# Kernel optimization log

Measured on AMD Instinct MI355X. Metric: run time of the kernel, lower is better.

The kernel has to match this reference:

```python
import jax, jax.numpy as jnp
import numpy as np
from functools import partial

ALPHA = 0.1
THETA = 0.5
N_NODES = 100000
N_EDGES = 3200000


def _gcn_norm(edge_index, num_nodes):
    # add self loops, compute symmetric normalization D^-1/2 (A+I) D^-1/2
    loops = jnp.arange(num_nodes, dtype=edge_index.dtype)
    src = jnp.concatenate([edge_index[0], loops])
    dst = jnp.concatenate([edge_index[1], loops])
    deg = jax.ops.segment_sum(jnp.ones_like(dst, dtype=jnp.float32), dst,
                              num_segments=num_nodes)
    dinv = jnp.where(deg > 0, jax.lax.rsqrt(deg), 0.0)
    norm = dinv[src] * dinv[dst]  # [E+N]
    return src, dst, norm


def _propagate(h, src, dst, norm, num_nodes):
    # out[i] = sum_{e: dst[e]=i} norm[e] * h[src[e]]
    msg = h[src] * norm[:, None]
    return jax.ops.segment_sum(msg, dst, num_segments=num_nodes)


def setup_inputs() -> dict:
    key = jax.random.key(0)
    ks = jax.random.split(key, 7)
    H, Fin, Fout, L = 256, 512, 64, 8
    x = jax.random.normal(ks[0], (N_NODES, Fin), dtype=jnp.float32)
    edge_index = jax.random.randint(ks[1], (2, N_EDGES), 0, N_NODES, dtype=jnp.int64)
    s = 1.0 / np.sqrt(Fin)
    W0 = jax.random.normal(ks[2], (Fin, H), dtype=jnp.float32) * s
    b0 = jax.random.normal(ks[3], (H,), dtype=jnp.float32) * 0.01
    Ws = jax.random.normal(ks[4], (L, H, H), dtype=jnp.float32) / np.sqrt(H)
    Wc = jax.random.normal(ks[5], (H, Fout), dtype=jnp.float32) / np.sqrt(H)
    bc = jax.random.normal(ks[6], (Fout,), dtype=jnp.float32) * 0.01
    return {"x": x, "edge_index": edge_index, "W0": W0, "b0": b0,
            "Ws": Ws, "Wc": Wc, "bc": bc}


def reference(x, edge_index, W0, b0, Ws, Wc, bc):
    num_nodes = x.shape[0]
    src, dst, norm = _gcn_norm(edge_index, num_nodes)
    # initial projection (dropout is identity in eval mode)
    x0 = jax.nn.relu(x @ W0 + b0)  # [N, H]
    h = x0
    layer_num = Ws.shape[0]
    for i in range(layer_num):
        beta = float(np.log(THETA / (i + 1) + 1.0))
        agg = _propagate(h, src, dst, norm, num_nodes)          # Ahat @ h
        z = (1.0 - ALPHA) * agg + ALPHA * x0                    # initial residual
        h = jax.nn.relu((1.0 - beta) * z + beta * (z @ Ws[i]))  # identity mapping
    embedding = h
    logits = embedding @ Wc + bc
    soft_label = jax.nn.softmax(logits, axis=1)
    hard_label = jnp.argmax(soft_label, axis=1)
    return logits, embedding, soft_label, hard_label
```

## Files before the change

### kernel.cpp

```cpp
#include <hip/hip_runtime.h>
#include <hip/hip_bf16.h>
#include <math.h>

#define NN   100000
#define FIN  512
#define HH   256
#define FOUT 64

typedef __attribute__((ext_vector_type(8))) short s16x8;
typedef __attribute__((ext_vector_type(4))) float f32x4;

__global__ void k_count(const int* __restrict__ dst, int* __restrict__ cnt, int E) {
    int i = blockIdx.x * 256 + threadIdx.x;
    if (i < E) atomicAdd(&cnt[dst[i]], 1);
}

__global__ void k_block_sums(const int* __restrict__ cnt, int* __restrict__ partial, int n) {
    __shared__ int red[256];
    int base = blockIdx.x * 1024;
    int t = threadIdx.x;
    int s = 0;
#pragma unroll
    for (int i = 0; i < 4; i++) { int idx = base + t * 4 + i; if (idx < n) s += cnt[idx]; }
    red[t] = s; __syncthreads();
    for (int off = 128; off > 0; off >>= 1) {
        if (t < off) red[t] += red[t + off];
        __syncthreads();
    }
    if (t == 0) partial[blockIdx.x] = red[0];
}

__global__ void k_scan_partials(int* partial, int nb, int* row_ptr, int n) {
    if (threadIdx.x == 0) {
        int run = 0;
        for (int i = 0; i < nb; i++) { int v = partial[i]; partial[i] = run; run += v; }
        row_ptr[n] = run;
    }
}

__global__ void k_write_rowptr(const int* __restrict__ cnt, const int* __restrict__ partial,
                               int* __restrict__ row_ptr, int* __restrict__ cur, int n) {
    __shared__ int sc[256];
    int base = blockIdx.x * 1024;
    int t = threadIdx.x;
    int v[4]; int s = 0;
#pragma unroll
    for (int i = 0; i < 4; i++) { int idx = base + t * 4 + i; v[i] = (idx < n) ? cnt[idx] : 0; s += v[i]; }
    sc[t] = s; __syncthreads();
    for (int off = 1; off < 256; off <<= 1) {
        int add = (t >= off) ? sc[t - off] : 0;
        __syncthreads();
        sc[t] += add;
        __syncthreads();
    }
    int run = partial[blockIdx.x] + sc[t] - s;
#pragma unroll
    for (int i = 0; i < 4; i++) {
        int idx = base + t * 4 + i;
        if (idx < n) { row_ptr[idx] = run; cur[idx] = run; run += v[i]; }
    }
}

__global__ void k_dinv(const int* __restrict__ cnt, float* __restrict__ dinv, int n) {
    int i = blockIdx.x * 256 + threadIdx.x;
    if (i < n) dinv[i] = 1.0f / sqrtf((float)(cnt[i] + 1));
}

__global__ void k_scatter(const int* __restrict__ src, const int* __restrict__ dst,
                          const float* __restrict__ dinv, int* __restrict__ cur,
                          int* __restrict__ src_sorted, float* __restrict__ norm_sorted, int E) {
    int i = blockIdx.x * 256 + threadIdx.x;
    if (i < E) {
        int s = src[i], d = dst[i];
        int p = atomicAdd(&cur[d], 1);
        src_sorted[p] = s;
        norm_sorted[p] = dinv[s] * dinv[d];
    }
}

__device__ __forceinline__ short f2bf_rn(float f) {
    unsigned b = __float_as_uint(f);
    unsigned r = b + 0x7FFFu + ((b >> 16) & 1u);
    return (short)(r >> 16);
}
__device__ __forceinline__ float bf2f(short h) {
    return __uint_as_float(((unsigned)(unsigned short)h) << 16);
}
__device__ __forceinline__ void split_bf16(float f, short& hi, short& lo) {
    hi = f2bf_rn(f);
    lo = f2bf_rn(f - bf2f(hi));
}

__global__ void k_wprep(const float* __restrict__ W, short* __restrict__ whi,
                        short* __restrict__ wlo, int K, float scale, int addId) {
    int t = blockIdx.x * 256 + threadIdx.x;
    int total = K * HH / 8;
    if (t >= total) return;
    int colin = t & 15, g = (t >> 4) & 3, nt = (t >> 6) & 15, kt = t >> 10;
    int col = nt * 16 + colin, kb = kt * 32 + g * 8;
    s16x8 h8, l8;
#pragma unroll
    for (int j = 0; j < 8; j++) {
        float f = scale * W[(size_t)(kb + j) * HH + col];
        if (addId && (kb + j) == col) f += 1.0f - scale;
        short h, l; split_bf16(f, h, l);
        h8[j] = h; l8[j] = l;
    }
    *(s16x8*)&whi[(size_t)t * 8] = h8;
    *(s16x8*)&wlo[(size_t)t * 8] = l8;
}

__global__ __launch_bounds__(256) void k_gemm0(
    const float* __restrict__ A, const short* __restrict__ Whi, const short* __restrict__ Wlo,
    const float* __restrict__ bias, float* __restrict__ C, int M) {
    __shared__ short As_hi[2][2048];
    __shared__ short As_lo[2][2048];
    int tid = threadIdx.x, lane = tid & 63, wid = tid >> 6;
    int wm = wid >> 1, wn = wid & 1;
    int bm = blockIdx.x * 64;
    int st_row = tid >> 2, st_g = tid & 3;
    int st_cphys = ((st_row & 15) ^ ((st_g & 1) << 2)) + 16 * st_g + 64 * (st_row >> 4);
    const float* st_ap = A + (size_t)(bm + st_row) * FIN + st_g * 8;
    bool st_ok = (bm + st_row) < M;
    int fr_g = lane >> 4, fr_r = lane & 15;
    int fr_base = (fr_r ^ ((fr_g & 1) << 2)) + 16 * fr_g;
    int c0 = (fr_base + 64 * (wm * 2 + 0)) * 8;
    int c1 = (fr_base + 64 * (wm * 2 + 1)) * 8;
    int lane_off = fr_g * 16 + fr_r;
    f32x4 acc[2][8] = {};
    f32x4 v0 = {0.f, 0.f, 0.f, 0.f}, v1 = v0, n0 = v0, n1 = v0;
    if (st_ok) { v0 = *(const f32x4*)(st_ap); v1 = *(const f32x4*)(st_ap + 4); }
    for (int kt = 0; kt < FIN / 32; kt++) {
        int buf = kt & 1;
        s16x8 h8, l8;
        {
            float fv[8] = {v0.x, v0.y, v0.z, v0.w, v1.x, v1.y, v1.z, v1.w};
#pragma unroll
            for (int j = 0; j < 8; j++) { short hh, ll; split_bf16(fv[j], hh, ll); h8[j] = hh; l8[j] = ll; }
        }
        *(s16x8*)&As_hi[buf][st_cphys * 8] = h8;
        *(s16x8*)&As_lo[buf][st_cphys * 8] = l8;
        if (kt + 1 < FIN / 32 && st_ok) {
            int k0n = (kt + 1) * 32;
            n0 = *(const f32x4*)(st_ap + k0n);
            n1 = *(const f32x4*)(st_ap + k0n + 4);
        }
        __syncthreads();
        s16x8 ah0 = *(const s16x8*)&As_hi[buf][c0], al0 = *(const s16x8*)&As_lo[buf][c0];
        s16x8 ah1 = *(const s16x8*)&As_hi[buf][c1], al1 = *(const s16x8*)&As_lo[buf][c1];
        size_t btile = (size_t)kt * 1024 + (size_t)(wn * 8) * 64;
#pragma unroll
        for (int ct = 0; ct < 8; ct++) {
            s16x8 bh = *(const s16x8*)&Whi[(btile + ct * 64 + lane_off) * 8];
            s16x8 bl = *(const s16x8*)&Wlo[(btile + ct * 64 + lane_off) * 8];
            acc[0][ct] = __builtin_amdgcn_mfma_f32_16x16x32_bf16(ah0, bh, acc[0][ct], 0, 0, 0);
            acc[0][ct] = __builtin_amdgcn_mfma_f32_16x16x32_bf16(al0, bh, acc[0][ct], 0, 0, 0);
            acc[0][ct] = __builtin_amdgcn_mfma_f32_16x16x32_bf16(ah0, bl, acc[0][ct], 0, 0, 0);
            acc[1][ct] = __builtin_amdgcn_mfma_f32_16x16x32_bf16(ah1, bh, acc[1][ct], 0, 0, 0);
            acc[1][ct] = __builtin_amdgcn_mfma_f32_16x16x32_bf16(al1, bh, acc[1][ct], 0, 0, 0);
            acc[1][ct] = __builtin_amdgcn_mfma_f32_16x16x32_bf16(ah1, bl, acc[1][ct], 0, 0, 0);
        }
        v0 = n0; v1 = n1;
    }
    int rsub = (lane >> 4) * 4, csub = lane & 15;
#pragma unroll
    for (int rt = 0; rt < 2; rt++)
#pragma unroll
        for (int ct = 0; ct < 8; ct++) {
            int col = wn * 128 + ct * 16 + csub;
            int r0 = bm + wm * 32 + rt * 16 + rsub;
#pragma unroll
            for (int reg = 0; reg < 4; reg++) {
                int row = r0 + reg;
                if (row < M) {
                    float o = fmaxf(acc[rt][ct][reg] + bias[col], 0.f);
                    C[(size_t)(col >> 7) * ((size_t)M * 128) + (size_t)row * 128 + (col & 127)] = o;
                }
            }
        }
}

__global__ __launch_bounds__(256) void k_prop(
    const float* __restrict__ hc, const float* __restrict__ x0c,
    const int* __restrict__ row_ptr, const int* __restrict__ src_sorted,
    const float* __restrict__ norm_sorted, const float* __restrict__ dinv,
    float* __restrict__ zc, int M) {
    int wid = threadIdx.x >> 6, lane = threadIdx.x & 63;
    int node = blockIdx.x * 4 + wid;
    if (node >= M) return;
    int slot = lane >> 5, f4 = (lane & 31) * 4;
    int e0 = __builtin_amdgcn_readfirstlane(row_ptr[node]);
    int e1 = __builtin_amdgcn_readfirstlane(row_ptr[node + 1]);
    f32x4 acc = {0.f, 0.f, 0.f, 0.f};
    int e = e0 + slot;
    for (; e + 2 < e1; e += 4) {
        int s0 = src_sorted[e];     float w0 = norm_sorted[e];
        int s1 = src_sorted[e + 2]; float w1 = norm_sorted[e + 2];
        f32x4 v0 = *(const f32x4*)&hc[(size_t)s0 * 128 + f4];
        f32x4 v1 = *(const f32x4*)&hc[(size_t)s1 * 128 + f4];
        acc += w0 * v0 + w1 * v1;
    }
    if (e < e1) {
        int s0 = src_sorted[e]; float w0 = norm_sorted[e];
        acc += w0 * (*(const f32x4*)&hc[(size_t)s0 * 128 + f4]);
    }
#pragma unroll
    for (int c = 0; c < 4; c++) acc[c] += __shfl_xor(acc[c], 32);
    float di = dinv[node], sw = di * di;
    size_t base = (size_t)node * 128 + f4;
    f32x4 hrow = *(const f32x4*)&hc[base];
    f32x4 xv = *(const f32x4*)&x0c[base];
    f32x4 z = 0.9f * (acc + sw * hrow) + 0.1f * xv;
    if (slot == 0) *(f32x4*)&zc[base] = z;
}

__global__ __launch_bounds__(256) void k_mgemm_z(
    const float* __restrict__ Zc, const short* __restrict__ Whi, const short* __restrict__ Wlo,
    float* __restrict__ C, int M, int rowmajor) {
    __shared__ short As_hi[2][2048];
    __shared__ short As_lo[2][2048];
    int tid = threadIdx.x, lane = tid & 63, wid = tid >> 6;
    int wm = wid >> 1, wn = wid & 1;
    int bm = blockIdx.x * 64;
    size_t CS = (size_t)M * 128;
    int st_row = tid >> 2, st_g = tid & 3;
    int st_cphys = ((st_row & 15) ^ ((st_g & 1) << 2)) + 16 * st_g + 64 * (st_row >> 4);
    bool st_ok = (bm + st_row) < M;
    int fr_g = lane >> 4, fr_r = lane & 15;
    int fr_base = (fr_r ^ ((fr_g & 1) << 2)) + 16 * fr_g;
    int c0 = (fr_base + 64 * (wm * 2 + 0)) * 8;
    int c1 = (fr_base + 64 * (wm * 2 + 1)) * 8;
    int lane_off = fr_g * 16 + fr_r;
    f32x4 acc[2][8] = {};
    auto zslab = [&](int kt) {
        int k0 = kt * 32;
        return Zc + (size_t)(k0 >> 7) * CS + (size_t)(bm + st_row) * 128 + (k0 & 127) + st_g * 8;
    };
    f32x4 v0 = {0.f, 0.f, 0.f, 0.f}, v1 = v0, n0 = v0, n1 = v0;
    if (st_ok) { const float* zp = zslab(0); v0 = *(const f32x4*)zp; v1 = *(const f32x4*)(zp + 4); }
    for (int kt = 0; kt < 8; kt++) {
        int buf = kt & 1;
        s16x8 h8, l8;
        {
            float fv[8] = {v0.x, v0.y, v0.z, v0.w, v1.x, v1.y, v1.z, v1.w};
#pragma unroll
            for (int j = 0; j < 8; j++) { short hh, ll; split_bf16(fv[j], hh, ll); h8[j] = hh; l8[j] = ll; }
        }
        *(s16x8*)&As_hi[buf][st_cphys * 8] = h8;
        *(s16x8*)&As_lo[buf][st_cphys * 8] = l8;
        if (kt + 1 < 8 && st_ok) {
            const float* zp = zslab(kt + 1);
            n0 = *(const f32x4*)zp; n1 = *(const f32x4*)(zp + 4);
        }
        __syncthreads();
        s16x8 ah0 = *(const s16x8*)&As_hi[buf][c0], al0 = *(const s16x8*)&As_lo[buf][c0];
        s16x8 ah1 = *(const s16x8*)&As_hi[buf][c1], al1 = *(const s16x8*)&As_lo[buf][c1];
        size_t btile = (size_t)kt * 1024 + (size_t)(wn * 8) * 64;
#pragma unroll
        for (int ct = 0; ct < 8; ct++) {
            s16x8 bh = *(const s16x8*)&Whi[(btile + ct * 64 + lane_off) * 8];
            s16x8 bl = *(const s16x8*)&Wlo[(btile + ct * 64 + lane_off) * 8];
            acc[0][ct] = __builtin_amdgcn_mfma_f32_16x16x32_bf16(ah0, bh, acc[0][ct], 0, 0, 0);
            acc[0][ct] = __builtin_amdgcn_mfma_f32_16x16x32_bf16(al0, bh, acc[0][ct], 0, 0, 0);
            acc[0][ct] = __builtin_amdgcn_mfma_f32_16x16x32_bf16(ah0, bl, acc[0][ct], 0, 0, 0);
            acc[1][ct] = __builtin_amdgcn_mfma_f32_16x16x32_bf16(ah1, bh, acc[1][ct], 0, 0, 0);
            acc[1][ct] = __builtin_amdgcn_mfma_f32_16x16x32_bf16(al1, bh, acc[1][ct], 0, 0, 0);
            acc[1][ct] = __builtin_amdgcn_mfma_f32_16x16x32_bf16(ah1, bl, acc[1][ct], 0, 0, 0);
        }
        v0 = n0; v1 = n1;
    }
    int rsub = (lane >> 4) * 4, csub = lane & 15;
#pragma unroll
    for (int rt = 0; rt < 2; rt++)
#pragma unroll
        for (int ct = 0; ct < 8; ct++) {
            int col = wn * 128 + ct * 16 + csub;
            int r0 = bm + wm * 32 + rt * 16 + rsub;
#pragma unroll
            for (int reg = 0; reg < 4; reg++) {
                int row = r0 + reg;
                if (row < M) {
                    float o = fmaxf(acc[rt][ct][reg], 0.f);
                    if (rowmajor) C[(size_t)row * HH + col] = o;
                    else C[(size_t)(col >> 7) * CS + (size_t)row * 128 + (col & 127)] = o;
                }
            }
        }
}

__global__ __launch_bounds__(256) void k_final2(
    const float* __restrict__ h, const float* __restrict__ Wc, const float* __restrict__ bc,
    float* __restrict__ logits, float* __restrict__ soft, float* __restrict__ hard, int M) {
    __shared__ float As[16][64];
    __shared__ float Bs[16][64];
    __shared__ float lg[64][64];
    int tid = threadIdx.x;
    int tx = tid & 15, ty = tid >> 4;
    int bm = blockIdx.x * 64;
    int lm = tid >> 2, lk = (tid & 3) * 4;
    int lkb = tid >> 4, lnb = (tid & 15) * 4;
    bool arow_ok = (bm + lm) < M;
    float acc[4][4] = {};
    for (int k0 = 0; k0 < HH; k0 += 16) {
        float4 av = make_float4(0.f, 0.f, 0.f, 0.f);
        if (arow_ok) av = *(const float4*)&h[(size_t)(bm + lm) * HH + k0 + lk];
        As[lk + 0][lm] = av.x; As[lk + 1][lm] = av.y; As[lk + 2][lm] = av.z; As[lk + 3][lm] = av.w;
        *(float4*)&Bs[lkb][lnb] = *(const float4*)&Wc[(size_t)(k0 + lkb) * FOUT + lnb];
        __syncthreads();
#pragma unroll
        for (int k = 0; k < 16; k++) {
            float4 a = *(const float4*)&As[k][ty * 4];
            float4 b = *(const float4*)&Bs[k][tx * 4];
            acc[0][0] += a.x * b.x; acc[0][1] += a.x * b.y; acc[0][2] += a.x * b.z; acc[0][3] += a.x * b.w;
            acc[1][0] += a.y * b.x; acc[1][1] += a.y * b.y; acc[1][2] += a.y * b.z; acc[1][3] += a.y * b.w;
            acc[2][0] += a.z * b.x; acc[2][1] += a.z * b.y; acc[2][2] += a.z * b.z; acc[2][3] += a.z * b.w;
            acc[3][0] += a.w * b.x; acc[3][1] += a.w * b.y; acc[3][2] += a.w * b.z; acc[3][3] += a.w * b.w;
        }
        __syncthreads();
    }
#pragma unroll
    for (int i = 0; i < 4; i++)
        *(float4*)&lg[ty * 4 + i][tx * 4] = make_float4(acc[i][0], acc[i][1], acc[i][2], acc[i][3]);
    __syncthreads();

    int wid = tid >> 6, lane = tid & 63;
    float bv = bc[lane];
    for (int r = wid * 16; r < wid * 16 + 16; r++) {
        int node = bm + r;
        if (node >= M) continue;
        float v = lg[r][lane] + bv;
        float m = v;
        for (int off = 32; off > 0; off >>= 1) m = fmaxf(m, __shfl_xor(m, off));
        float ev = expf(v - m);
        float s = ev;
        for (int off = 32; off > 0; off >>= 1) s += __shfl_xor(s, off);
        float sm = ev / s;
        int idx = lane; float vv = v;
        for (int off = 1; off < 64; off <<= 1) {
            float ov = __shfl_xor(vv, off);
            int oi = __shfl_xor(idx, off);
            if (ov > vv || (ov == vv && oi < idx)) { vv = ov; idx = oi; }
        }
        logits[(size_t)node * FOUT + lane] = v;
        soft[(size_t)node * FOUT + lane] = sm;
        if (lane == 0) hard[node] = (float)idx;
    }
}

extern "C" void kernel_launch(void* const* d_in, const int* in_sizes, int n_in,
                              void* d_out, int out_size, void* d_ws, size_t ws_size,
                              hipStream_t stream) {
    const float* x  = (const float*)d_in[0];
    const int*   ei = (const int*)d_in[1];
    const float* W0 = (const float*)d_in[2];
    const float* b0 = (const float*)d_in[3];
    const float* Ws = (const float*)d_in[4];
    const float* Wc = (const float*)d_in[5];
    const float* bc = (const float*)d_in[6];
    const int E = in_sizes[1] / 2;
    const int N = in_sizes[0] / FIN;
    const int L = in_sizes[4] / (HH * HH);

    float* out    = (float*)d_out;
    float* logits = out;
    float* emb    = out + (size_t)N * FOUT;
    float* soft   = emb + (size_t)N * HH;
    float* hard   = soft + (size_t)N * FOUT;

    char* p = (char*)d_ws;
    size_t off = 0;
    auto alloc = [&](size_t bytes) { void* r = p + off; off += (bytes + 255) & ~(size_t)255; return r; };
    int*   cnt         = (int*)alloc((size_t)N * 4);
    int*   row_ptr     = (int*)alloc((size_t)(N + 1) * 4);
    int*   cur         = (int*)alloc((size_t)N * 4);
    int*   partial     = (int*)alloc(4096 * 4);
    float* dinv        = (float*)alloc((size_t)N * 4);
    int*   src_sorted  = (int*)alloc((size_t)E * 4);
    float* norm_sorted = (float*)alloc((size_t)E * 4);
    float* X0c         = (float*)alloc((size_t)N * HH * 4);
    float* hAc         = (float*)alloc((size_t)N * HH * 4);
    float* hBc         = (float*)alloc((size_t)N * HH * 4);
    short* W0hi        = (short*)alloc((size_t)FIN * HH * 2);
    short* W0lo        = (short*)alloc((size_t)FIN * HH * 2);
    short* Wshi        = (short*)alloc((size_t)L * HH * HH * 2);
    short* Wslo        = (short*)alloc((size_t)L * HH * HH * 2);

    const int* srcp = ei;
    const int* dstp = ei + E;
    const size_t CS = (size_t)N * 128;

    hipMemsetAsync(cnt, 0, (size_t)N * 4, stream);
    k_count<<<(E + 255) / 256, 256, 0, stream>>>(dstp, cnt, E);
    const int nb = (N + 1023) / 1024;
    k_block_sums<<<nb, 256, 0, stream>>>(cnt, partial, N);
    k_scan_partials<<<1, 64, 0, stream>>>(partial, nb, row_ptr, N);
    k_write_rowptr<<<nb, 256, 0, stream>>>(cnt, partial, row_ptr, cur, N);
    k_dinv<<<(N + 255) / 256, 256, 0, stream>>>(cnt, dinv, N);
    k_scatter<<<(E + 255) / 256, 256, 0, stream>>>(srcp, dstp, dinv, cur, src_sorted, norm_sorted, E);

    k_wprep<<<(FIN * HH / 8 + 255) / 256, 256, 0, stream>>>(W0, W0hi, W0lo, FIN, 1.0f, 0);
    for (int i = 0; i < L; i++) {
        float beta = (float)log(0.5 / (i + 1) + 1.0);
        k_wprep<<<(HH * HH / 8 + 255) / 256, 256, 0, stream>>>(
            Ws + (size_t)i * HH * HH, Wshi + (size_t)i * HH * HH, Wslo + (size_t)i * HH * HH,
            HH, beta, 1);
    }

    const int nblk = (N + 63) / 64;
    const int npb  = (N + 3) / 4;
    k_gemm0<<<nblk, 256, 0, stream>>>(x, W0hi, W0lo, b0, X0c, N);

    const float* hsrc = X0c;
    for (int i = 0; i < L; i++) {
        int last = (i == L - 1);
        float* hdst = last ? emb : ((i & 1) ? hBc : hAc);
        float* zb = last ? hBc : hdst;
        for (int c = 0; c < 2; c++)
            k_prop<<<npb, 256, 0, stream>>>(hsrc + c * CS, X0c + c * CS, row_ptr,
                                            src_sorted, norm_sorted, dinv, zb + c * CS, N);
        k_mgemm_z<<<nblk, 256, 0, stream>>>(zb, Wshi + (size_t)i * HH * HH, Wslo + (size_t)i * HH * HH,
                                            hdst, N, last);
        hsrc = hdst;
    }
    k_final2<<<nblk, 256, 0, stream>>>(emb, Wc, bc, logits, soft, hard, N);
}
```

Measured before the change: 4.995 ms.

## Split GEMM tiles across 8 waves and batch weight prep into one launch

The two MFMA GEMM kernels go from 256 to 512 threads per block, so each wave owns a 32x64 output slice instead of 32x128, halving its accumulator registers. Only the first 256 threads stage A into shared memory, and a second barrier per k-step is added to protect the double buffer. The per-layer weight-prep launches are merged into one kernel that computes beta on the device. The aim is more waves in flight and fewer launches, at the cost of extra barriers and idle staging threads.

After: 4.840 ms. 1.03x faster.

```diff
diff --git a/kernel.cpp b/kernel.cpp
--- a/kernel.cpp
+++ b/kernel.cpp
@@ -92,7 +92,7 @@
 }
 
 __global__ void k_wprep(const float* __restrict__ W, short* __restrict__ whi,
-                        short* __restrict__ wlo, int K, float scale, int addId) {
+                        short* __restrict__ wlo, int K) {
     int t = blockIdx.x * 256 + threadIdx.x;
     int total = K * HH / 8;
     if (t >= total) return;
@@ -101,8 +101,7 @@
     s16x8 h8, l8;
 #pragma unroll
     for (int j = 0; j < 8; j++) {
-        float f = scale * W[(size_t)(kb + j) * HH + col];
-        if (addId && (kb + j) == col) f += 1.0f - scale;
+        float f = W[(size_t)(kb + j) * HH + col];
         short h, l; split_bf16(f, h, l);
         h8[j] = h; l8[j] = l;
     }
@@ -110,47 +109,70 @@
     *(s16x8*)&wlo[(size_t)t * 8] = l8;
 }
 
-__global__ __launch_bounds__(256) void k_gemm0(
+__global__ void k_wprep_all(const float* __restrict__ Ws, short* __restrict__ whi,
+                            short* __restrict__ wlo, int L) {
+    int t = blockIdx.x * 256 + threadIdx.x;
+    const int per = HH * HH / 8;
+    if (t >= L * per) return;
+    int layer = t / per;
+    int tl = t - layer * per;
+    float beta = (float)log(0.5 / (layer + 1) + 1.0);
+    const float* W = Ws + (size_t)layer * HH * HH;
+    int colin = tl & 15, g = (tl >> 4) & 3, nt = (tl >> 6) & 15, kt = tl >> 10;
+    int col = nt * 16 + colin, kb = kt * 32 + g * 8;
+    s16x8 h8, l8;
+#pragma unroll
+    for (int j = 0; j < 8; j++) {
+        float f = beta * W[(size_t)(kb + j) * HH + col];
+        if ((kb + j) == col) f += 1.0f - beta;
+        short h, l; split_bf16(f, h, l);
+        h8[j] = h; l8[j] = l;
+    }
+    *(s16x8*)&whi[(size_t)t * 8] = h8;
+    *(s16x8*)&wlo[(size_t)t * 8] = l8;
+}
+
+__global__ __launch_bounds__(512, 4) void k_gemm0(
     const float* __restrict__ A, const short* __restrict__ Whi, const short* __restrict__ Wlo,
     const float* __restrict__ bias, float* __restrict__ C, int M) {
     __shared__ short As_hi[2][2048];
     __shared__ short As_lo[2][2048];
     int tid = threadIdx.x, lane = tid & 63, wid = tid >> 6;
-    int wm = wid >> 1, wn = wid & 1;
+    int wm = wid >> 2, wn = wid & 3;
     int bm = blockIdx.x * 64;
     int st_row = tid >> 2, st_g = tid & 3;
     int st_cphys = ((st_row & 15) ^ ((st_g & 1) << 2)) + 16 * st_g + 64 * (st_row >> 4);
     const float* st_ap = A + (size_t)(bm + st_row) * FIN + st_g * 8;
-    bool st_ok = (bm + st_row) < M;
+    bool st_ok = (tid < 256) && (bm + st_row) < M;
     int fr_g = lane >> 4, fr_r = lane & 15;
     int fr_base = (fr_r ^ ((fr_g & 1) << 2)) + 16 * fr_g;
     int c0 = (fr_base + 64 * (wm * 2 + 0)) * 8;
     int c1 = (fr_base + 64 * (wm * 2 + 1)) * 8;
     int lane_off = fr_g * 16 + fr_r;
-    f32x4 acc[2][8] = {};
+    f32x4 acc[2][4] = {};
     f32x4 v0 = {0.f, 0.f, 0.f, 0.f}, v1 = v0, n0 = v0, n1 = v0;
     if (st_ok) { v0 = *(const f32x4*)(st_ap); v1 = *(const f32x4*)(st_ap + 4); }
     for (int kt = 0; kt < FIN / 32; kt++) {
         int buf = kt & 1;
-        s16x8 h8, l8;
-        {
+        if (tid < 256) {
+            s16x8 h8, l8;
             float fv[8] = {v0.x, v0.y, v0.z, v0.w, v1.x, v1.y, v1.z, v1.w};
 #pragma unroll
             for (int j = 0; j < 8; j++) { short hh, ll; split_bf16(fv[j], hh, ll); h8[j] = hh; l8[j] = ll; }
-        }
-        *(s16x8*)&As_hi[buf][st_cphys * 8] = h8;
-        *(s16x8*)&As_lo[buf][st_cphys * 8] = l8;
-        if (kt + 1 < FIN / 32 && st_ok) {
-            int k0n = (kt + 1) * 32;
-            n0 = *(const f32x4*)(st_ap + k0n);
-            n1 = *(const f32x4*)(st_ap + k0n + 4);
+            *(s16x8*)&As_hi[buf][st_cphys * 8] = h8;
+            *(s16x8*)&As_lo[buf][st_cphys * 8] = l8;
+            if (kt + 1 < FIN / 32 && st_ok) {
+                int k0n = (kt + 1) * 32;
+                n0 = *(const f32x4*)(st_ap + k0n);
+                n1 = *(const f32x4*)(st_ap + k0n + 4);
+            }
         }
         __syncthreads();
         s16x8 ah0 = *(const s16x8*)&As_hi[buf][c0], al0 = *(const s16x8*)&As_lo[buf][c0];
         s16x8 ah1 = *(const s16x8*)&As_hi[buf][c1], al1 = *(const s16x8*)&As_lo[buf][c1];
-        size_t btile = (size_t)kt * 1024 + (size_t)(wn * 8) * 64;
-#pragma unroll
-        for (int ct = 0; ct < 8; ct++) {
+        size_t btile = (size_t)kt * 1024 + (size_t)(wn * 4) * 64;
+#pragma unroll
+        for (int ct = 0; ct < 4; ct++) {
             s16x8 bh = *(const s16x8*)&Whi[(btile + ct * 64 + lane_off) * 8];
             s16x8 bl = *(const s16x8*)&Wlo[(btile + ct * 64 + lane_off) * 8];
             acc[0][ct] = __builtin_amdgcn_mfma_f32_16x16x32_bf16(ah0, bh, acc[0][ct], 0, 0, 0);
@@ -161,13 +183,14 @@
             acc[1][ct] = __builtin_amdgcn_mfma_f32_16x16x32_bf16(ah1, bl, acc[1][ct], 0, 0, 0);
         }
         v0 = n0; v1 = n1;
+        if (kt + 1 < FIN / 32) __syncthreads();
     }
     int rsub = (lane >> 4) * 4, csub = lane & 15;
 #pragma unroll
     for (int rt = 0; rt < 2; rt++)
 #pragma unroll
-        for (int ct = 0; ct < 8; ct++) {
-            int col = wn * 128 + ct * 16 + csub;
+        for (int ct = 0; ct < 4; ct++) {
+            int col = wn * 64 + ct * 16 + csub;
             int r0 = bm + wm * 32 + rt * 16 + rsub;
 #pragma unroll
             for (int reg = 0; reg < 4; reg++) {
@@ -214,24 +237,24 @@
     if (slot == 0) *(f32x4*)&zc[base] = z;
 }
 
-__global__ __launch_bounds__(256) void k_mgemm_z(
+__global__ __launch_bounds__(512, 4) void k_mgemm_z(
     const float* __restrict__ Zc, const short* __restrict__ Whi, const short* __restrict__ Wlo,
     float* __restrict__ C, int M, int rowmajor) {
     __shared__ short As_hi[2][2048];
     __shared__ short As_lo[2][2048];
     int tid = threadIdx.x, lane = tid & 63, wid = tid >> 6;
-    int wm = wid >> 1, wn = wid & 1;
+    int wm = wid >> 2, wn = wid & 3;
     int bm = blockIdx.x * 64;
     size_t CS = (size_t)M * 128;
     int st_row = tid >> 2, st_g = tid & 3;
+    bool st_ok = (tid < 256) && (bm + st_row) < M;
     int st_cphys = ((st_row & 15) ^ ((st_g & 1) << 2)) + 16 * st_g + 64 * (st_row >> 4);
-    bool st_ok = (bm + st_row) < M;
     int fr_g = lane >> 4, fr_r = lane & 15;
     int fr_base = (fr_r ^ ((fr_g & 1) << 2)) + 16 * fr_g;
     int c0 = (fr_base + 64 * (wm * 2 + 0)) * 8;
     int c1 = (fr_base + 64 * (wm * 2 + 1)) * 8;
     int lane_off = fr_g * 16 + fr_r;
-    f32x4 acc[2][8] = {};
+    f32x4 acc[2][4] = {};
     auto zslab = [&](int kt) {
         int k0 = kt * 32;
         return Zc + (size_t)(k0 >> 7) * CS + (size_t)(bm + st_row) * 128 + (k0 & 127) + st_g * 8;
@@ -240,24 +263,24 @@
     if (st_ok) { const float* zp = zslab(0); v0 = *(const f32x4*)zp; v1 = *(const f32x4*)(zp + 4); }
     for (int kt = 0; kt < 8; kt++) {
         int buf = kt & 1;
-        s16x8 h8, l8;
-        {
+        if (tid < 256) {
+            s16x8 h8, l8;
             float fv[8] = {v0.x, v0.y, v0.z, v0.w, v1.x, v1.y, v1.z, v1.w};
 #pragma unroll
             for (int j = 0; j < 8; j++) { short hh, ll; split_bf16(fv[j], hh, ll); h8[j] = hh; l8[j] = ll; }
-        }
-        *(s16x8*)&As_hi[buf][st_cphys * 8] = h8;
-        *(s16x8*)&As_lo[buf][st_cphys * 8] = l8;
-        if (kt + 1 < 8 && st_ok) {
-            const float* zp = zslab(kt + 1);
-            n0 = *(const f32x4*)zp; n1 = *(const f32x4*)(zp + 4);
+            *(s16x8*)&As_hi[buf][st_cphys * 8] = h8;
+            *(s16x8*)&As_lo[buf][st_cphys * 8] = l8;
+            if (kt + 1 < 8 && st_ok) {
+                const float* zp = zslab(kt + 1);
+                n0 = *(const f32x4*)zp; n1 = *(const f32x4*)(zp + 4);
+            }
         }
         __syncthreads();
         s16x8 ah0 = *(const s16x8*)&As_hi[buf][c0], al0 = *(const s16x8*)&As_lo[buf][c0];
         s16x8 ah1 = *(const s16x8*)&As_hi[buf][c1], al1 = *(const s16x8*)&As_lo[buf][c1];
-        size_t btile = (size_t)kt * 1024 + (size_t)(wn * 8) * 64;
-#pragma unroll
-        for (int ct = 0; ct < 8; ct++) {
+        size_t btile = (size_t)kt * 1024 + (size_t)(wn * 4) * 64;
+#pragma unroll
+        for (int ct = 0; ct < 4; ct++) {
             s16x8 bh = *(const s16x8*)&Whi[(btile + ct * 64 + lane_off) * 8];
             s16x8 bl = *(const s16x8*)&Wlo[(btile + ct * 64 + lane_off) * 8];
             acc[0][ct] = __builtin_amdgcn_mfma_f32_16x16x32_bf16(ah0, bh, acc[0][ct], 0, 0, 0);
@@ -268,13 +291,14 @@
             acc[1][ct] = __builtin_amdgcn_mfma_f32_16x16x32_bf16(ah1, bl, acc[1][ct], 0, 0, 0);
         }
         v0 = n0; v1 = n1;
+        if (kt + 1 < 8) __syncthreads();
     }
     int rsub = (lane >> 4) * 4, csub = lane & 15;
 #pragma unroll
     for (int rt = 0; rt < 2; rt++)
 #pragma unroll
-        for (int ct = 0; ct < 8; ct++) {
-            int col = wn * 128 + ct * 16 + csub;
+        for (int ct = 0; ct < 4; ct++) {
+            int col = wn * 64 + ct * 16 + csub;
             int r0 = bm + wm * 32 + rt * 16 + rsub;
 #pragma unroll
             for (int reg = 0; reg < 4; reg++) {
@@ -398,17 +422,12 @@
     k_dinv<<<(N + 255) / 256, 256, 0, stream>>>(cnt, dinv, N);
     k_scatter<<<(E + 255) / 256, 256, 0, stream>>>(srcp, dstp, dinv, cur, src_sorted, norm_sorted, E);
 
-    k_wprep<<<(FIN * HH / 8 + 255) / 256, 256, 0, stream>>>(W0, W0hi, W0lo, FIN, 1.0f, 0);
-    for (int i = 0; i < L; i++) {
-        float beta = (float)log(0.5 / (i + 1) + 1.0);
-        k_wprep<<<(HH * HH / 8 + 255) / 256, 256, 0, stream>>>(
-            Ws + (size_t)i * HH * HH, Wshi + (size_t)i * HH * HH, Wslo + (size_t)i * HH * HH,
-            HH, beta, 1);
-    }
+    k_wprep<<<(FIN * HH / 8 + 255) / 256, 256, 0, stream>>>(W0, W0hi, W0lo, FIN);
+    k_wprep_all<<<(L * HH * HH / 8 + 255) / 256, 256, 0, stream>>>(Ws, Wshi, Wslo, L);
 
     const int nblk = (N + 63) / 64;
     const int npb  = (N + 3) / 4;
-    k_gemm0<<<nblk, 256, 0, stream>>>(x, W0hi, W0lo, b0, X0c, N);
+    k_gemm0<<<nblk, 512, 0, stream>>>(x, W0hi, W0lo, b0, X0c, N);
 
     const float* hsrc = X0c;
     for (int i = 0; i < L; i++) {
@@ -418,7 +437,7 @@
         for (int c = 0; c < 2; c++)
             k_prop<<<npb, 256, 0, stream>>>(hsrc + c * CS, X0c + c * CS, row_ptr,
                                             src_sorted, norm_sorted, dinv, zb + c * CS, N);
-        k_mgemm_z<<<nblk, 256, 0, stream>>>(zb, Wshi + (size_t)i * HH * HH, Wslo + (size_t)i * HH * HH,
+        k_mgemm_z<<<nblk, 512, 0, stream>>>(zb, Wshi + (size_t)i * HH * HH, Wslo + (size_t)i * HH * HH,
                                             hdst, N, last);
         hsrc = hdst;
     }
```
